# Optimization experiments

Measured on AMD Instinct MI355X. Metric: run time of the kernel, lower is better.

Reference implementation:

```python
import jax, jax.numpy as jnp
import numpy as np

B = 4096      # graphs per batch
V = 32        # vertices per graph
F = 16        # num_atom_types (input node features)
NB = 8        # num_bond_types (edge feature dim)
C = 128       # conv_dim
E_PER = 256   # random edges per graph
NEG_SLOPE = 0.2


def setup_inputs() -> dict:
    rng = np.random.default_rng(0)
    N = B * V
    # random intra-graph edges (duplicates are fine; softmax handles them)
    off = (np.arange(B, dtype=np.int64) * V)[:, None]
    src = (rng.integers(0, V, (B, E_PER)) + off).ravel()
    dst = (rng.integers(0, V, (B, E_PER)) + off).ravel()
    bond = rng.integers(0, NB, src.shape[0])
    eattr = np.zeros((src.shape[0], NB), dtype=np.float32)
    eattr[np.arange(src.shape[0]), bond] = 1.0
    # self loops with edge_attr = per-target-node mean (PyG fill_value='mean')
    sums = np.zeros((N, NB), dtype=np.float64)
    np.add.at(sums, dst, eattr)
    cnt = np.bincount(dst, minlength=N).astype(np.float64)
    loop_attr = (sums / np.maximum(cnt, 1.0)[:, None]).astype(np.float32)
    loops = np.arange(N, dtype=np.int64)
    edge_index = np.stack([np.concatenate([src, loops]),
                           np.concatenate([dst, loops])])  # [2, E]
    edge_attr = np.concatenate([eattr, loop_attr], axis=0)  # [E, NB]

    key = jax.random.key(0)
    ks = jax.random.split(key, 8)
    inp = {
        "x": jax.random.normal(ks[0], (N, F), jnp.float32),
        "edge_index": jnp.asarray(edge_index),
        "edge_attr": jnp.asarray(edge_attr),
        "W_lin": jax.random.normal(ks[1], (F, C), jnp.float32) / np.sqrt(F),
        "att_src": jax.random.normal(ks[2], (C,), jnp.float32) / np.sqrt(C),
        "att_dst": jax.random.normal(ks[3], (C,), jnp.float32) / np.sqrt(C),
        "att_edge": jax.random.normal(ks[4], (C,), jnp.float32) / np.sqrt(C),
        "W_edge": jax.random.normal(ks[5], (NB, C), jnp.float32) / np.sqrt(NB),
        "b_gat": jnp.zeros((C,), jnp.float32),
        "W_out": jax.random.normal(ks[6], (C, 1), jnp.float32) / np.sqrt(C),
        "b_out": jnp.zeros((1,), jnp.float32),
        "num_graphs": B,
    }
    return inp


def reference(x, edge_index, edge_attr, W_lin, att_src, att_dst, att_edge,
              W_edge, b_gat, W_out, b_out, num_graphs):
    N = x.shape[0]
    src, dst = edge_index[0], edge_index[1]
    h = x @ W_lin                           # [N, C] node transform
    a_src = h @ att_src                     # [N]
    a_dst = h @ att_dst                     # [N]
    a_edge = (edge_attr @ W_edge) @ att_edge  # [E]
    alpha = jax.nn.leaky_relu(a_src[src] + a_dst[dst] + a_edge, NEG_SLOPE)
    # segment softmax over incoming edges of each dst node
    m = jax.ops.segment_max(alpha, dst, num_segments=N)
    m = jnp.where(jnp.isfinite(m), m, 0.0)
    ex = jnp.exp(alpha - m[dst])
    denom = jax.ops.segment_sum(ex, dst, num_segments=N)
    w = ex / denom[dst]                     # [E] attention weights
    msg = h[src] * w[:, None]               # [E, C]
    out_nodes = jax.ops.segment_sum(msg, dst, num_segments=N) + b_gat  # [N, C]
    gf = out_nodes.reshape(num_graphs, -1, out_nodes.shape[-1]).mean(axis=1)  # [B, C]
    out = gf @ W_out + b_out                # [B, 1]
    return (out, gf)
```

## Files before the change

kernel.cpp:

```cpp
#include <hip/hip_runtime.h>


#define BB   4096
#define VV   32
#define FF   16
#define NBB  8
#define CC   128
#define EPER 256
constexpr int NTOT  = BB * VV;
constexpr int ERAND = BB * EPER;
constexpr int ETOT  = ERAND + NTOT;
constexpr float SLOPE = 0.2f;

__device__ __forceinline__ unsigned f2key(float f) {
  unsigned u = __float_as_uint(f);
  return (u & 0x80000000u) ? ~u : (u | 0x80000000u);
}
__device__ __forceinline__ float key2f(unsigned k) {
  unsigned u = (k & 0x80000000u) ? (k & 0x7fffffffu) : ~k;
  return __uint_as_float(u);
}

__launch_bounds__(256, 4)
__global__ void gnn_fused(const float* __restrict__ x,
                          const int*   __restrict__ eidx,
                          const float* __restrict__ eattr,
                          const float* __restrict__ W_lin,
                          const float* __restrict__ att_src,
                          const float* __restrict__ att_dst,
                          const float* __restrict__ att_edge,
                          const float* __restrict__ W_edge,
                          const float* __restrict__ b_gat,
                          const float* __restrict__ W_out,
                          const float* __restrict__ b_out,
                          float* __restrict__ out,
                          float* __restrict__ gf_out)
{
  const int g    = blockIdx.x;
  const int t    = threadIdx.x;
  const int lane = t & 63;
  const int wave = __builtin_amdgcn_readfirstlane((int)threadIdx.x) >> 6;

  __shared__ float    s_asrc[VV], s_adst[VV];
  __shared__ unsigned s_mkey[VV];
  __shared__ float    s_denom[VV], s_inv[VV], s_r[VV];
  __shared__ float    s_we[NBB];
  __shared__ float    s_gp[4][CC];
  __shared__ float    s_gf[CC];

  if (t < VV) { s_mkey[t] = 0u; s_denom[t] = 0.f; s_r[t] = 0.f; }

  int e_sl, e_dl;
  float4 ea0, ea1;
  {
    const int ge = g * EPER + t;
    e_sl = eidx[ge] - g * VV;
    e_dl = eidx[ETOT + ge] - g * VV;
    const float4* ap = (const float4*)(eattr + (size_t)ge * NBB);
    ea0 = ap[0]; ea1 = ap[1];
  }
  float4 la0 = {0,0,0,0}, la1 = {0,0,0,0};
  if (t < VV) {
    const float4* ap = (const float4*)(eattr + (size_t)(ERAND + g * VV + t) * NBB);
    la0 = ap[0]; la1 = ap[1];
  }

  {
    const int f = t >> 5;
    const int j = t & 31;
    float p = 0.f;
    #pragma unroll
    for (int k = 0; k < 4; ++k)
      p += W_edge[f * CC + j + 32 * k] * att_edge[j + 32 * k];
    #pragma unroll
    for (int m = 1; m <= 16; m <<= 1) p += __shfl_xor(p, m);
    if (j == 0) s_we[f] = p;
  }

  const float2* W2 = (const float2*)W_lin;
  float2 wcol[FF];
  #pragma unroll
  for (int f = 0; f < FF; ++f) wcol[f] = W2[f * (CC / 2) + lane];
  const float2 as2 = ((const float2*)att_src)[lane];
  const float2 ad2 = ((const float2*)att_dst)[lane];

  const float* xg = x + (size_t)g * VV * FF;
  float h0[8], h1[8];
  #pragma unroll
  for (int dv = 0; dv < 8; ++dv) {
    const int v = wave * 8 + dv;
    const float* xr = xg + v * FF;
    float a0 = 0.f, a1 = 0.f;
    #pragma unroll
    for (int f = 0; f < FF; ++f) {
      const float xv = xr[f];
      a0 += xv * wcol[f].x;
      a1 += xv * wcol[f].y;
    }
    h0[dv] = a0; h1[dv] = a1;
    float ps = a0 * as2.x + a1 * as2.y;
    float pd = a0 * ad2.x + a1 * ad2.y;
    #pragma unroll
    for (int m = 1; m <= 32; m <<= 1) {
      ps += __shfl_xor(ps, m);
      pd += __shfl_xor(pd, m);
    }
    if (lane == 0) { s_asrc[v] = ps; s_adst[v] = pd; }
  }
  __syncthreads();

  float e_alpha, l_alpha = 0.f;
  {
    const float aed = ea0.x*s_we[0] + ea0.y*s_we[1] + ea0.z*s_we[2] + ea0.w*s_we[3]
                    + ea1.x*s_we[4] + ea1.y*s_we[5] + ea1.z*s_we[6] + ea1.w*s_we[7];
    float a = s_asrc[e_sl] + s_adst[e_dl] + aed;
    e_alpha = a > 0.f ? a : SLOPE * a;
    atomicMax(&s_mkey[e_dl], f2key(e_alpha));
  }
  if (t < VV) {
    const float aed = la0.x*s_we[0] + la0.y*s_we[1] + la0.z*s_we[2] + la0.w*s_we[3]
                    + la1.x*s_we[4] + la1.y*s_we[5] + la1.z*s_we[6] + la1.w*s_we[7];
    float a = s_asrc[t] + s_adst[t] + aed;
    l_alpha = a > 0.f ? a : SLOPE * a;
    atomicMax(&s_mkey[t], f2key(l_alpha));
  }
  __syncthreads();

  const float e_ex = __expf(e_alpha - key2f(s_mkey[e_dl]));
  atomicAdd(&s_denom[e_dl], e_ex);
  float l_ex = 0.f;
  if (t < VV) {
    l_ex = __expf(l_alpha - key2f(s_mkey[t]));
    atomicAdd(&s_denom[t], l_ex);
  }
  __syncthreads();
  if (t < VV) s_inv[t] = 1.0f / s_denom[t];
  __syncthreads();

  atomicAdd(&s_r[e_sl], e_ex * s_inv[e_dl]);
  if (t < VV) atomicAdd(&s_r[t], l_ex * s_inv[t]);
  __syncthreads();

  float p0 = 0.f, p1 = 0.f;
  #pragma unroll
  for (int dv = 0; dv < 8; ++dv) {
    const float rv = s_r[wave * 8 + dv];
    p0 += rv * h0[dv];
    p1 += rv * h1[dv];
  }
  ((float2*)(&s_gp[wave][0]))[lane] = make_float2(p0, p1);
  __syncthreads();

  if (t < CC) {
    const float gf = (s_gp[0][t] + s_gp[1][t] + s_gp[2][t] + s_gp[3][t]) * (1.0f / VV)
                   + b_gat[t];
    gf_out[(size_t)g * CC + t] = gf;
    s_gf[t] = gf;
  }
  __syncthreads();

  if (t < 64) {
    float p = s_gf[t] * W_out[t] + s_gf[t + 64] * W_out[t + 64];
    #pragma unroll
    for (int m = 32; m >= 1; m >>= 1) p += __shfl_xor(p, m);
    if (t == 0) out[g] = p + b_out[0];
  }
}

extern "C" void kernel_launch(void* const* d_in, const int* in_sizes, int n_in,
                              void* d_out, int out_size, void* d_ws, size_t ws_size,
                              hipStream_t stream) {
  const float* x        = (const float*)d_in[0];
  const int*   eidx     = (const int*)  d_in[1];
  const float* eattr    = (const float*)d_in[2];
  const float* W_lin    = (const float*)d_in[3];
  const float* att_src  = (const float*)d_in[4];
  const float* att_dst  = (const float*)d_in[5];
  const float* att_edge = (const float*)d_in[6];
  const float* W_edge   = (const float*)d_in[7];
  const float* b_gat    = (const float*)d_in[8];
  const float* W_out    = (const float*)d_in[9];
  const float* b_out    = (const float*)d_in[10];

  float* out = (float*)d_out;
  float* gf  = out + BB;

  gnn_fused<<<dim3(BB), dim3(256), 0, stream>>>(
      x, eidx, eattr, W_lin, att_src, att_dst, att_edge, W_edge,
      b_gat, W_out, b_out, out, gf);
}
```

Measured before the change: 142.1 us.

## Fold attention vectors into weights and process one graph per wavefront

A tiny precompute kernel folds att_src/att_dst into W_lin and att_edge into W_edge, so node attention scores come from a 16-wide dot product on x instead of the full 128-wide h. The main kernel maps one graph per wave (four graphs per block), so block-wide barriers become wave-local fences. It reassociates the output as (sum_v r_v x_v) @ W_lin, which removes the per-node h computation. The costs are an extra launch, reliance on wave-synchronous shared-memory ordering, and a different floating-point summation order.

```diff
diff --git a/kernel.cpp b/kernel.cpp
--- a/kernel.cpp
+++ b/kernel.cpp
@@ -21,150 +21,162 @@
   return __uint_as_float(u);
 }
 
+__launch_bounds__(64)
+__global__ void gnn_precompute(const float* __restrict__ W_lin,
+                               const float* __restrict__ att_src,
+                               const float* __restrict__ att_dst,
+                               const float* __restrict__ W_edge,
+                               const float* __restrict__ att_edge,
+                               float* __restrict__ ws)
+{
+  const int l = threadIdx.x;
+  const float2 as = ((const float2*)att_src)[l];
+  const float2 ad = ((const float2*)att_dst)[l];
+  const float2 ae = ((const float2*)att_edge)[l];
+  #pragma unroll
+  for (int f = 0; f < FF; ++f) {
+    const float2 w = ((const float2*)W_lin)[f * 64 + l];
+    float ps = w.x * as.x + w.y * as.y;
+    float pd = w.x * ad.x + w.y * ad.y;
+    #pragma unroll
+    for (int m = 1; m <= 32; m <<= 1) { ps += __shfl_xor(ps, m); pd += __shfl_xor(pd, m); }
+    if (l == 0) { ws[f] = ps; ws[FF + f] = pd; }
+  }
+  #pragma unroll
+  for (int f = 0; f < NBB; ++f) {
+    const float2 w = ((const float2*)W_edge)[f * 64 + l];
+    float pe = w.x * ae.x + w.y * ae.y;
+    #pragma unroll
+    for (int m = 1; m <= 32; m <<= 1) pe += __shfl_xor(pe, m);
+    if (l == 0) ws[2 * FF + f] = pe;
+  }
+}
+
 __launch_bounds__(256, 4)
-__global__ void gnn_fused(const float* __restrict__ x,
-                          const int*   __restrict__ eidx,
-                          const float* __restrict__ eattr,
-                          const float* __restrict__ W_lin,
-                          const float* __restrict__ att_src,
-                          const float* __restrict__ att_dst,
-                          const float* __restrict__ att_edge,
-                          const float* __restrict__ W_edge,
-                          const float* __restrict__ b_gat,
-                          const float* __restrict__ W_out,
-                          const float* __restrict__ b_out,
-                          float* __restrict__ out,
-                          float* __restrict__ gf_out)
+__global__ void gnn_main(const float* __restrict__ x,
+                         const int*   __restrict__ eidx,
+                         const float* __restrict__ eattr,
+                         const float* __restrict__ W_lin,
+                         const float* __restrict__ b_gat,
+                         const float* __restrict__ W_out,
+                         const float* __restrict__ b_out,
+                         const float* __restrict__ ws,
+                         float* __restrict__ out,
+                         float* __restrict__ gf_out)
 {
-  const int g    = blockIdx.x;
   const int t    = threadIdx.x;
   const int lane = t & 63;
-  const int wave = __builtin_amdgcn_readfirstlane((int)threadIdx.x) >> 6;
-
-  __shared__ float    s_asrc[VV], s_adst[VV];
-  __shared__ unsigned s_mkey[VV];
-  __shared__ float    s_denom[VV], s_inv[VV], s_r[VV];
-  __shared__ float    s_we[NBB];
-  __shared__ float    s_gp[4][CC];
-  __shared__ float    s_gf[CC];
-
-  if (t < VV) { s_mkey[t] = 0u; s_denom[t] = 0.f; s_r[t] = 0.f; }
-
-  int e_sl, e_dl;
-  float4 ea0, ea1;
-  {
-    const int ge = g * EPER + t;
-    e_sl = eidx[ge] - g * VV;
-    e_dl = eidx[ETOT + ge] - g * VV;
+  const int wave = __builtin_amdgcn_readfirstlane(t) >> 6;
+  const int g    = blockIdx.x * 4 + wave;
+
+  __shared__ float    s_asrc[4][VV], s_adst[4][VV];
+  __shared__ unsigned s_mkey[4][VV];
+  __shared__ float    s_den[4][VV];
+  __shared__ float    s_r[4][VV];
+  __shared__ float    s_xt[4][FF * 33];
+
+  if (lane < VV) { s_mkey[wave][lane] = 0u; s_den[wave][lane] = 0.f; s_r[wave][lane] = 0.f; }
+
+  int es[4], ed[4];
+  float4 ea0[4], ea1[4];
+  const int gbase = g * EPER;
+  #pragma unroll
+  for (int k = 0; k < 4; ++k) {
+    const int ge = gbase + 64 * k + lane;
+    es[k] = eidx[ge] - g * VV;
+    ed[k] = eidx[ETOT + ge] - g * VV;
     const float4* ap = (const float4*)(eattr + (size_t)ge * NBB);
-    ea0 = ap[0]; ea1 = ap[1];
+    ea0[k] = ap[0]; ea1[k] = ap[1];
   }
   float4 la0 = {0,0,0,0}, la1 = {0,0,0,0};
-  if (t < VV) {
-    const float4* ap = (const float4*)(eattr + (size_t)(ERAND + g * VV + t) * NBB);
+  if (lane < VV) {
+    const float4* ap = (const float4*)(eattr + (size_t)(ERAND + g * VV + lane) * NBB);
     la0 = ap[0]; la1 = ap[1];
   }
 
-  {
-    const int f = t >> 5;
-    const int j = t & 31;
-    float p = 0.f;
-    #pragma unroll
-    for (int k = 0; k < 4; ++k)
-      p += W_edge[f * CC + j + 32 * k] * att_edge[j + 32 * k];
-    #pragma unroll
-    for (int m = 1; m <= 16; m <<= 1) p += __shfl_xor(p, m);
-    if (j == 0) s_we[f] = p;
-  }
-
+  float xr[FF] = {};
+  if (lane < VV) {
+    const float* xp = x + (size_t)(g * VV + lane) * FF;
+    #pragma unroll
+    for (int f = 0; f < FF; ++f) xr[f] = xp[f];
+    float a0 = 0.f, a1 = 0.f;
+    #pragma unroll
+    for (int f = 0; f < FF; ++f) { a0 += xr[f] * ws[f]; a1 += xr[f] * ws[FF + f]; }
+    s_asrc[wave][lane] = a0; s_adst[wave][lane] = a1;
+  }
+  __threadfence_block();
+
+  float al[5];
+  #pragma unroll
+  for (int k = 0; k < 4; ++k) {
+    const float aed = ea0[k].x*ws[32] + ea0[k].y*ws[33] + ea0[k].z*ws[34] + ea0[k].w*ws[35]
+                    + ea1[k].x*ws[36] + ea1[k].y*ws[37] + ea1[k].z*ws[38] + ea1[k].w*ws[39];
+    const float a = s_asrc[wave][es[k]] + s_adst[wave][ed[k]] + aed;
+    al[k] = a > 0.f ? a : SLOPE * a;
+    atomicMax(&s_mkey[wave][ed[k]], f2key(al[k]));
+  }
+  al[4] = 0.f;
+  if (lane < VV) {
+    const float aed = la0.x*ws[32] + la0.y*ws[33] + la0.z*ws[34] + la0.w*ws[35]
+                    + la1.x*ws[36] + la1.y*ws[37] + la1.z*ws[38] + la1.w*ws[39];
+    const float a = s_asrc[wave][lane] + s_adst[wave][lane] + aed;
+    al[4] = a > 0.f ? a : SLOPE * a;
+    atomicMax(&s_mkey[wave][lane], f2key(al[4]));
+  }
+  __threadfence_block();
+
+  float ex[5];
+  #pragma unroll
+  for (int k = 0; k < 4; ++k) {
+    ex[k] = __expf(al[k] - key2f(s_mkey[wave][ed[k]]));
+    atomicAdd(&s_den[wave][ed[k]], ex[k]);
+  }
+  ex[4] = 0.f;
+  if (lane < VV) {
+    ex[4] = __expf(al[4] - key2f(s_mkey[wave][lane]));
+    atomicAdd(&s_den[wave][lane], ex[4]);
+  }
+  __threadfence_block();
+  if (lane < VV) s_den[wave][lane] = 1.0f / s_den[wave][lane];
+  __threadfence_block();
+
+  #pragma unroll
+  for (int k = 0; k < 4; ++k)
+    atomicAdd(&s_r[wave][es[k]], ex[k] * s_den[wave][ed[k]]);
+  if (lane < VV)
+    atomicAdd(&s_r[wave][lane], ex[4] * s_den[wave][lane]);
+  __threadfence_block();
+
+  if (lane < VV) {
+    const float rl = s_r[wave][lane];
+    #pragma unroll
+    for (int f = 0; f < FF; ++f) s_xt[wave][f * 33 + lane] = xr[f] * rl;
+  }
+  __threadfence_block();
+  const int fy = lane & 15, part = lane >> 4;
+  float yp = 0.f;
+  #pragma unroll
+  for (int j = 0; j < 8; ++j) yp += s_xt[wave][fy * 33 + part * 8 + j];
+  yp += __shfl_xor(yp, 16);
+  yp += __shfl_xor(yp, 32);
+  yp *= (1.0f / VV);
+
+  const float2 bg = ((const float2*)b_gat)[lane];
+  float gx = bg.x, gy = bg.y;
   const float2* W2 = (const float2*)W_lin;
-  float2 wcol[FF];
-  #pragma unroll
-  for (int f = 0; f < FF; ++f) wcol[f] = W2[f * (CC / 2) + lane];
-  const float2 as2 = ((const float2*)att_src)[lane];
-  const float2 ad2 = ((const float2*)att_dst)[lane];
-
-  const float* xg = x + (size_t)g * VV * FF;
-  float h0[8], h1[8];
-  #pragma unroll
-  for (int dv = 0; dv < 8; ++dv) {
-    const int v = wave * 8 + dv;
-    const float* xr = xg + v * FF;
-    float a0 = 0.f, a1 = 0.f;
-    #pragma unroll
-    for (int f = 0; f < FF; ++f) {
-      const float xv = xr[f];
-      a0 += xv * wcol[f].x;
-      a1 += xv * wcol[f].y;
-    }
-    h0[dv] = a0; h1[dv] = a1;
-    float ps = a0 * as2.x + a1 * as2.y;
-    float pd = a0 * ad2.x + a1 * ad2.y;
-    #pragma unroll
-    for (int m = 1; m <= 32; m <<= 1) {
-      ps += __shfl_xor(ps, m);
-      pd += __shfl_xor(pd, m);
-    }
-    if (lane == 0) { s_asrc[v] = ps; s_adst[v] = pd; }
-  }
-  __syncthreads();
-
-  float e_alpha, l_alpha = 0.f;
-  {
-    const float aed = ea0.x*s_we[0] + ea0.y*s_we[1] + ea0.z*s_we[2] + ea0.w*s_we[3]
-                    + ea1.x*s_we[4] + ea1.y*s_we[5] + ea1.z*s_we[6] + ea1.w*s_we[7];
-    float a = s_asrc[e_sl] + s_adst[e_dl] + aed;
-    e_alpha = a > 0.f ? a : SLOPE * a;
-    atomicMax(&s_mkey[e_dl], f2key(e_alpha));
-  }
-  if (t < VV) {
-    const float aed = la0.x*s_we[0] + la0.y*s_we[1] + la0.z*s_we[2] + la0.w*s_we[3]
-                    + la1.x*s_we[4] + la1.y*s_we[5] + la1.z*s_we[6] + la1.w*s_we[7];
-    float a = s_asrc[t] + s_adst[t] + aed;
-    l_alpha = a > 0.f ? a : SLOPE * a;
-    atomicMax(&s_mkey[t], f2key(l_alpha));
-  }
-  __syncthreads();
-
-  const float e_ex = __expf(e_alpha - key2f(s_mkey[e_dl]));
-  atomicAdd(&s_denom[e_dl], e_ex);
-  float l_ex = 0.f;
-  if (t < VV) {
-    l_ex = __expf(l_alpha - key2f(s_mkey[t]));
-    atomicAdd(&s_denom[t], l_ex);
-  }
-  __syncthreads();
-  if (t < VV) s_inv[t] = 1.0f / s_denom[t];
-  __syncthreads();
-
-  atomicAdd(&s_r[e_sl], e_ex * s_inv[e_dl]);
-  if (t < VV) atomicAdd(&s_r[t], l_ex * s_inv[t]);
-  __syncthreads();
-
-  float p0 = 0.f, p1 = 0.f;
-  #pragma unroll
-  for (int dv = 0; dv < 8; ++dv) {
-    const float rv = s_r[wave * 8 + dv];
-    p0 += rv * h0[dv];
-    p1 += rv * h1[dv];
-  }
-  ((float2*)(&s_gp[wave][0]))[lane] = make_float2(p0, p1);
-  __syncthreads();
-
-  if (t < CC) {
-    const float gf = (s_gp[0][t] + s_gp[1][t] + s_gp[2][t] + s_gp[3][t]) * (1.0f / VV)
-                   + b_gat[t];
-    gf_out[(size_t)g * CC + t] = gf;
-    s_gf[t] = gf;
-  }
-  __syncthreads();
-
-  if (t < 64) {
-    float p = s_gf[t] * W_out[t] + s_gf[t + 64] * W_out[t + 64];
-    #pragma unroll
-    for (int m = 32; m >= 1; m >>= 1) p += __shfl_xor(p, m);
-    if (t == 0) out[g] = p + b_out[0];
-  }
+  #pragma unroll
+  for (int f = 0; f < FF; ++f) {
+    const float yf = __shfl(yp, f);
+    const float2 w = W2[f * 64 + lane];
+    gx += yf * w.x; gy += yf * w.y;
+  }
+  ((float2*)(gf_out + (size_t)g * CC))[lane] = make_float2(gx, gy);
+
+  const float2 wo = ((const float2*)W_out)[lane];
+  float p = gx * wo.x + gy * wo.y;
+  #pragma unroll
+  for (int m = 1; m <= 32; m <<= 1) p += __shfl_xor(p, m);
+  if (lane == 0) out[g] = p + b_out[0];
 }
 
 extern "C" void kernel_launch(void* const* d_in, const int* in_sizes, int n_in,
@@ -182,10 +194,12 @@
   const float* W_out    = (const float*)d_in[9];
   const float* b_out    = (const float*)d_in[10];
 
+  float* ws  = (float*)d_ws;
   float* out = (float*)d_out;
   float* gf  = out + BB;
 
-  gnn_fused<<<dim3(BB), dim3(256), 0, stream>>>(
-      x, eidx, eattr, W_lin, att_src, att_dst, att_edge, W_edge,
-      b_gat, W_out, b_out, out, gf);
-}
+  gnn_precompute<<<dim3(1), dim3(64), 0, stream>>>(W_lin, att_src, att_dst,
+                                                   W_edge, att_edge, ws);
+  gnn_main<<<dim3(BB / 4), dim3(256), 0, stream>>>(
+      x, eidx, eattr, W_lin, b_gat, W_out, b_out, ws, out, gf);
+}
```

After: 128.2 us. 9.8% less time.
